# Optimization experiments

Measured on AMD Instinct MI355X. Metric: run time of the kernel, lower is better.

Reference implementation:

```python
import jax, jax.numpy as jnp
import numpy as np

RADIUS = 0.1
NSAMPLE = 32
NUM_KP = 15
KP_EXTENT = 1.0
DENSITY_PARAM = 5.0
EXTENT = 2.0 * KP_EXTENT * RADIUS / DENSITY_PARAM  # 0.04
K_RADIUS = 1.5 * EXTENT                            # 0.06
C_IN, C_OUT = 64, 128
BN_EPS = 1e-5


def make_kernel_points():
    # Deterministic stand-in for create_kernel_points: first point at center
    # ('center' fixed mode), remaining points quasi-uniform in a ball of K_RADIUS.
    rs = np.random.RandomState(0)
    d = rs.randn(NUM_KP - 1, 3)
    d /= np.linalg.norm(d, axis=1, keepdims=True) + 1e-9
    r = rs.rand(NUM_KP - 1, 1) ** (1.0 / 3.0)
    pts = np.concatenate([np.zeros((1, 3)), d * r * K_RADIUS], axis=0)
    return jnp.asarray(pts, dtype=jnp.float32)  # [K, 3]


def ball_group(query_xyz, support_xyz, support_mask, radius, nsample):
    """Masked ordered ball query. Returns idx [B,N1,S] int32 and mask [B,N1,S] float."""
    # [B, N1, N2] squared distances (dominant memory traffic)
    d2 = jnp.sum((query_xyz[:, :, None, :] - support_xyz[:, None, :, :]) ** 2, axis=-1)
    valid = (d2 < radius * radius) & (support_mask[:, None, :] > 0)
    order = jnp.cumsum(valid.astype(jnp.int32), axis=-1) - 1  # rank among valid, per row
    in_cap = valid & (order < nsample)
    slot = jnp.where(in_cap, order, nsample)  # overflow -> dump slot
    B, N1, N2 = d2.shape
    j = jnp.broadcast_to(jnp.arange(N2, dtype=jnp.int32), (B, N1, N2))
    b = jnp.arange(B)[:, None, None]
    n = jnp.arange(N1)[None, :, None]
    idx = jnp.zeros((B, N1, nsample + 1), jnp.int32).at[b, n, slot].set(j)[..., :nsample]
    cnt = jnp.sum(in_cap.astype(jnp.int32), axis=-1)  # [B, N1]
    nb_mask = jnp.arange(nsample)[None, None, :] < cnt[:, :, None]
    idx = jnp.where(nb_mask, idx, idx[:, :, :1])  # pad with first neighbor
    return idx, nb_mask.astype(jnp.float32)


def setup_inputs() -> dict:
    key = jax.random.key(0)
    ks = jax.random.split(key, 6)
    B, N1, N2 = 4, 2048, 8192
    query_xyz = jax.random.uniform(ks[0], (B, N1, 3), dtype=jnp.float32)
    support_xyz = jax.random.uniform(ks[1], (B, N2, 3), dtype=jnp.float32)
    query_mask = jnp.ones((B, N1), jnp.float32)
    support_mask = jnp.ones((B, N2), jnp.float32)
    support_features = jax.random.normal(ks[2], (B, C_IN, N2), dtype=jnp.float32)
    kernel_weights = jax.random.normal(ks[3], (NUM_KP, C_IN), dtype=jnp.float32) * (1.0 / np.sqrt(C_IN))
    W_out = jax.random.normal(ks[4], (C_OUT, C_IN), dtype=jnp.float32) * (1.0 / np.sqrt(C_IN))
    gamma = jnp.ones((C_OUT,), jnp.float32)
    beta = jnp.zeros((C_OUT,), jnp.float32)
    return {
        "query_xyz": query_xyz, "support_xyz": support_xyz,
        "query_mask": query_mask, "support_mask": support_mask,
        "support_features": support_features, "K_points": make_kernel_points(),
        "kernel_weights": kernel_weights, "W_out": W_out,
        "gamma": gamma, "beta": beta,
    }


def reference(query_xyz, support_xyz, query_mask, support_mask, support_features,
              K_points, kernel_weights, W_out, gamma, beta):
    idx, nb_mask = ball_group(query_xyz, support_xyz, support_mask, RADIUS, NSAMPLE)
    # gather neighbor features: [B, N2, C] -> [B, N1, S, C]
    feats_t = jnp.transpose(support_features, (0, 2, 1))
    nbr_feats = jnp.take_along_axis(feats_t[:, None, :, :],
                                    idx[:, :, :, None], axis=2)  # [B,N1,S,C]
    # grouped relative positions: [B, N1, S, 3]
    grouped_xyz = jnp.take_along_axis(support_xyz[:, None, :, :],
                                      idx[:, :, :, None], axis=2)
    rel_pos = grouped_xyz - query_xyz[:, :, None, :]
    # kernel-point distances: [B, N1, S, K]
    diff = rel_pos[:, :, :, None, :] - K_points[None, None, None, :, :]
    sq_d = jnp.sum(diff * diff, axis=-1)
    # linear influence, then permute to [B, N1, K, S]
    w = jnp.clip(1.0 - jnp.sqrt(sq_d) / EXTENT, 0.0, None)
    w = jnp.transpose(w, (0, 1, 3, 2))
    feature_mask = nb_mask + (1.0 - query_mask[:, :, None])  # [B,N1,S]
    w = w * feature_mask[:, :, None, :]
    # weighted sum over neighbors: [B, N1, K, C]
    weighted = jnp.einsum('bnks,bnsc->bnkc', w, nbr_feats)
    out = jnp.sum(weighted * kernel_weights[None, None, :, :], axis=2)  # [B,N1,C]
    out = jnp.transpose(out, (0, 2, 1))  # [B, C_in, N1]
    # out_conv: 1x1 conv (no bias) + BatchNorm1d (training-mode batch stats) + ReLU
    out = jnp.einsum('oc,bcn->bon', W_out, out)  # [B, C_out, N1]
    mean = jnp.mean(out, axis=(0, 2), keepdims=True)
    var = jnp.mean((out - mean) ** 2, axis=(0, 2), keepdims=True)
    out = (out - mean) * jax.lax.rsqrt(var + BN_EPS)
    out = out * gamma[None, :, None] + beta[None, :, None]
    return jax.nn.relu(out)
```

## Files before the change

### kernel.cpp

```cpp
#include <hip/hip_runtime.h>
#include <stdint.h>
#include <limits.h>

#define BATCH 4
#define N1D   2048
#define N2D   8192
#define NSAMP 32
#define NKP   15
#define CIN   64
#define COUT  128

#define RAD2    0.01f
#define INV_EXT 25.0f
#define BN_EPS  1e-5f
#define CMARG   0.1000001f

#define NWAVE 4
#define QPB   NWAVE
#define NCELL 1000
#define MAXC  80
#define NPF   4

#define WS_BPTS   131072
#define WS_FEATT  262144
#define WS_OUT2   2367488
#define WS_CS     3416064
#define WS_CNT    3420160
#define WS_CUR    3424256

__device__ __forceinline__ int cell_of(float x, float y, float z) {
  int cx = (int)(x*10.f); cx = cx < 0 ? 0 : (cx > 9 ? 9 : cx);
  int cy = (int)(y*10.f); cy = cy < 0 ? 0 : (cy > 9 ? 9 : cy);
  int cz = (int)(z*10.f); cz = cz < 0 ? 0 : (cz > 9 ? 9 : cz);
  return (cx*10 + cy)*10 + cz;
}

__global__ __launch_bounds__(256) void pg_prep(
    const float* __restrict__ sxyz, const float* __restrict__ smask,
    const float* __restrict__ sfeat, float* __restrict__ featT,
    int* __restrict__ cellCnt)
{
  __shared__ float tile[64*65];
  const int t  = threadIdx.x;
  const int bt = blockIdx.x;

  if (bt >= 512) {
    const int idx = bt - 512;
    const int bb  = idx >> 5;
    const int i   = ((idx & 31) << 8) + t;
    if (smask[bb*N2D + i] > 0.f) {
      const float* p = sxyz + ((size_t)bb*N2D + i)*3;
      atomicAdd(&cellCnt[bb*1024 + cell_of(p[0], p[1], p[2])], 1);
    }
    return;
  }

  const int b  = bt >> 7;
  const int j0 = (bt & 127) * 64;
  const float* src = sfeat + (size_t)(b*CIN)*N2D + j0;
#pragma unroll
  for (int i = 0; i < 4; ++i) {
    const int c  = i*16 + (t >> 4);
    const int j4 = (t & 15) * 4;
    const float4 v = *(const float4*)(src + (size_t)c*N2D + j4);
    tile[c*65 + j4+0] = v.x;
    tile[c*65 + j4+1] = v.y;
    tile[c*65 + j4+2] = v.z;
    tile[c*65 + j4+3] = v.w;
  }
  __syncthreads();
  float* dstb = featT + (size_t)(b*N2D + j0) * CIN;
#pragma unroll
  for (int r = 0; r < 4; ++r) {
    const int j  = r*16 + (t >> 4);
    const int c4 = (t & 15) * 4;
    float4 v;
    v.x = tile[(c4+0)*65 + j];
    v.y = tile[(c4+1)*65 + j];
    v.z = tile[(c4+2)*65 + j];
    v.w = tile[(c4+3)*65 + j];
    *(float4*)(dstb + j*CIN + c4) = v;
  }
}

__global__ __launch_bounds__(256) void pg_binscan(
    const int* __restrict__ cellCnt, const float* __restrict__ sxyz,
    const float* __restrict__ smask, int* __restrict__ cellCur,
    float4* __restrict__ bpts, int* __restrict__ cellStart)
{
  __shared__ int off_s[NCELL+1];
  __shared__ int wsum[4];
  const int t     = threadIdx.x;
  const int lane  = t & 63;
  const int wv    = t >> 6;
  const int bb    = blockIdx.x >> 5;
  const int slice = blockIdx.x & 31;
  const int* cnt  = cellCnt + bb*1024;

  int c0 = 0, c1 = 0, c2 = 0, c3 = 0, v = 0;
  if (t < 250) {
    c0 = cnt[t*4+0]; c1 = cnt[t*4+1]; c2 = cnt[t*4+2]; c3 = cnt[t*4+3];
    v = c0 + c1 + c2 + c3;
  }
  int x = v;
#pragma unroll
  for (int off = 1; off < 64; off <<= 1) {
    int y = __shfl_up(x, off);
    if (lane >= off) x += y;
  }
  if (lane == 63) wsum[wv] = x;
  __syncthreads();
  int base = 0;
#pragma unroll
  for (int w = 0; w < 4; ++w) if (w < wv) base += wsum[w];
  const int excl = base + x - v;
  if (t < 250) {
    int o = excl;
    off_s[t*4+0] = o; o += c0;
    off_s[t*4+1] = o; o += c1;
    off_s[t*4+2] = o; o += c2;
    off_s[t*4+3] = o;
  }
  if (t == 0) off_s[NCELL] = wsum[0]+wsum[1]+wsum[2]+wsum[3];
  __syncthreads();

  if (slice == 0) {
    for (int i = t; i < NCELL+1; i += 256)
      cellStart[bb*(NCELL+1) + i] = off_s[i];
  }

  const int i = slice*256 + t;
  if (smask[bb*N2D + i] > 0.f) {
    const float* p = sxyz + ((size_t)bb*N2D + i)*3;
    const float px = p[0], py = p[1], pz = p[2];
    const int cell = cell_of(px, py, pz);
    const int pos = off_s[cell] + atomicAdd(&cellCur[bb*1024 + cell], 1);
    bpts[(size_t)bb*N2D + pos] = make_float4(px, py, pz, __int_as_float(i));
  }
}

__global__ __launch_bounds__(256) void pg_main(
    const float* __restrict__ qxyz, const float* __restrict__ qmask,
    const float4* __restrict__ bpts, const int* __restrict__ cellStart,
    const float* __restrict__ featT, const float* __restrict__ Kp,
    const float* __restrict__ KW, const float* __restrict__ Wout,
    const float* __restrict__ sxyz, float* __restrict__ out2)
{
  __shared__ __align__(16) float4 s_cand4[QPB][MAXC];
  __shared__ __align__(16) int    s_candj[QPB][MAXC];
  __shared__ __align__(16) float4 s_sel[QPB][NSAMP];
  __shared__ __align__(16) int    s_j[QPB][NSAMP];
  __shared__ __align__(16) float  s_w[QPB*NSAMP*16];
  __shared__ float                s_xq[QPB*68];

  const int t    = threadIdx.x;
  const int lane = t & 63;
  const int wv   = t >> 6;
  const int gbase = blockIdx.x * QPB;
  const int b     = gbase >> 11;
  const uint64_t lt = (1ull << lane) - 1ull;

  const int g = gbase + wv;
  const float qx = qxyz[g*3+0], qy = qxyz[g*3+1], qz = qxyz[g*3+2];

  const float4* bptsb = bpts + (size_t)b*N2D;
  int cq;
  {
    int cx0 = (int)((qx-CMARG)*10.f); if (cx0 < 0) cx0 = 0;
    int cx1 = (int)((qx+CMARG)*10.f); if (cx1 > 9) cx1 = 9;
    int cy0 = (int)((qy-CMARG)*10.f); if (cy0 < 0) cy0 = 0;
    int cy1 = (int)((qy+CMARG)*10.f); if (cy1 > 9) cy1 = 9;
    int cz0 = (int)((qz-CMARG)*10.f); if (cz0 < 0) cz0 = 0;
    int cz1 = (int)((qz+CMARG)*10.f); if (cz1 > 9) cz1 = 9;
    const int ny = cy1 - cy0 + 1;
    const int npair = (cx1 - cx0 + 1) * ny;

    int len = 0, rs = 0;
    if (lane < npair) {
      const int cx = cx0 + lane / ny;
      const int cy = cy0 + lane % ny;
      const float lox = cx*0.1f, loy = cy*0.1f;
      const float dxc = fmaxf(fmaxf(lox - qx, qx - (lox+0.1f)), 0.f);
      const float dyc = fmaxf(fmaxf(loy - qy, qy - (loy+0.1f)), 0.f);
      if (dxc*dxc + dyc*dyc < RAD2) {
        const int* csb = cellStart + b*(NCELL+1) + (cx*10 + cy)*10;
        rs  = csb[cz0];
        len = csb[cz1 + 1] - rs;
      }
    }
    int pc = len;
#pragma unroll
    for (int off = 1; off < 16; off <<= 1) {
      int y = __shfl_up(pc, off);
      if (lane >= off) pc += y;
    }
    const int tot   = __shfl(pc, 15);
    const int excl  = pc - len;
    const int sbase = rs - excl;

    int segc[9], segb[9];
#pragma unroll
    for (int e = 0; e < 9; ++e) {
      const int ce = __builtin_amdgcn_readlane(excl,  e);
      const int be = __builtin_amdgcn_readlane(sbase, e);
      segc[e] = (e < npair) ? ce : INT_MAX;
      segb[e] = (e < npair) ? be : 0;
    }

    int ccnt = 0;
    for (int base0 = 0; base0 < tot; base0 += 64*NPF) {
      float4 pt[NPF];
#pragma unroll
      for (int u = 0; u < NPF; ++u) {
        const int idx = base0 + u*64 + lane;
        if (idx < tot) {
          int bb2 = segb[0];
#pragma unroll
          for (int e = 1; e < 9; ++e) if (segc[e] <= idx) bb2 = segb[e];
          pt[u] = bptsb[bb2 + idx];
        }
      }
#pragma unroll
      for (int u = 0; u < NPF; ++u) {
        const int idx = base0 + u*64 + lane;
        bool ok = false;
        if (idx < tot) {
          const float dx = pt[u].x - qx, dy = pt[u].y - qy, dz = pt[u].z - qz;
          ok = (dx*dx + dy*dy + dz*dz) < RAD2;
        }
        const uint64_t m = __ballot(ok);
        if (ok) {
          const int pos = ccnt + __popcll(m & lt);
          if (pos < MAXC) {
            s_cand4[wv][pos] = pt[u];
            s_candj[wv][pos] = __float_as_int(pt[u].w);
          }
        }
        ccnt += (int)__popcll(m);
      }
    }
    const int C = ccnt < MAXC ? ccnt : MAXC;
    const int C4 = (C + 3) & ~3;
    if (C + lane < C4) s_candj[wv][C + lane] = INT_MAX;

    const int jA = (lane      < C) ? s_candj[wv][lane]      : INT_MAX;
    const int jB = (lane + 64 < C) ? s_candj[wv][lane + 64] : INT_MAX;
    int rA = 0, rB = 0;
    for (int e = 0; e < C4; e += 4) {
      const int4 v4 = *(const int4*)&s_candj[wv][e];
      rA += (v4.x < jA) + (v4.y < jA) + (v4.z < jA) + (v4.w < jA);
      rB += (v4.x < jB) + (v4.y < jB) + (v4.z < jB) + (v4.w < jB);
    }
    if (lane      < C && rA < NSAMP) s_sel[wv][rA] = s_cand4[wv][lane];
    if (lane + 64 < C && rB < NSAMP) s_sel[wv][rB] = s_cand4[wv][lane + 64];
    cq = C < NSAMP ? C : NSAMP;
  }

  {
    const int s    = lane & 31;
    const int half = lane >> 5;
    float4 sel;
    if (cq > 0) {
      sel = s_sel[wv][s < cq ? s : 0];
    } else {
      sel = make_float4(sxyz[(size_t)b*N2D*3+0], sxyz[(size_t)b*N2D*3+1],
                        sxyz[(size_t)b*N2D*3+2], __int_as_float(0));
    }
    if (half == 0) s_j[wv][s] = __float_as_int(sel.w);
    const float rx = sel.x - qx;
    const float ry = sel.y - qy;
    const float rz = sel.z - qz;

    float w[8];
#pragma unroll
    for (int ki = 0; ki < 8; ++ki) {
      const int k  = half*8 + ki;
      const int kc = k < NKP-1 ? k : NKP-1;
      const float dx = rx - Kp[kc*3+0];
      const float dy = ry - Kp[kc*3+1];
      const float dz = rz - Kp[kc*3+2];
      float wk = fmaxf(1.0f - sqrtf(dx*dx+dy*dy+dz*dz)*INV_EXT, 0.0f);
      w[ki] = (k < NKP) ? wk : 0.0f;
    }
    float4* wrow = (float4*)&s_w[(wv*NSAMP + s)*16 + half*8];
    wrow[0] = make_float4(w[0], w[1], w[2], w[3]);
    wrow[1] = make_float4(w[4], w[5], w[6], w[7]);
  }

  {
    float kw[16];
#pragma unroll
    for (int k = 0; k < NKP; ++k) kw[k] = KW[k*CIN + lane];
    kw[15] = 0.0f;

    const float fpad = 1.0f - qmask[g];
    const int cqs = __builtin_amdgcn_readfirstlane(cq);

    float ft[NSAMP];
#pragma unroll
    for (int s = 0; s < NSAMP; ++s) {
      const int j = __builtin_amdgcn_readfirstlane(s_j[wv][s]);
      ft[s] = featT[(size_t)(b*N2D + j)*CIN + lane];
    }

    float acc = 0.0f;
#pragma unroll
    for (int s = 0; s < NSAMP; ++s) {
      const float fm = ((s < cqs) ? 1.0f : 0.0f) + fpad;
      const float4* wp = (const float4*)&s_w[(wv*NSAMP + s)*16];
      const float4 w0 = wp[0], w1 = wp[1], w2 = wp[2], w3 = wp[3];
      float wsum;
      wsum = w0.x*kw[0];
      wsum = fmaf(w0.y, kw[1],  wsum);
      wsum = fmaf(w0.z, kw[2],  wsum);
      wsum = fmaf(w0.w, kw[3],  wsum);
      wsum = fmaf(w1.x, kw[4],  wsum);
      wsum = fmaf(w1.y, kw[5],  wsum);
      wsum = fmaf(w1.z, kw[6],  wsum);
      wsum = fmaf(w1.w, kw[7],  wsum);
      wsum = fmaf(w2.x, kw[8],  wsum);
      wsum = fmaf(w2.y, kw[9],  wsum);
      wsum = fmaf(w2.z, kw[10], wsum);
      wsum = fmaf(w2.w, kw[11], wsum);
      wsum = fmaf(w3.x, kw[12], wsum);
      wsum = fmaf(w3.y, kw[13], wsum);
      wsum = fmaf(w3.z, kw[14], wsum);
      wsum = fmaf(w3.w, kw[15], wsum);
      acc = fmaf(fm*wsum, ft[s], acc);
    }
    s_xq[wv*68 + lane] = acc;
  }
  __syncthreads();

  {
    const int n4 = t & 3;
    const int og = t >> 2;
    const int gq = gbase + n4;
    const int nn = gq & 2047;
    const float4* xr = (const float4*)&s_xq[n4*68];
    const float4* w0 = (const float4*)(Wout + (og*2+0)*CIN);
    const float4* w1 = (const float4*)(Wout + (og*2+1)*CIN);
    float a0 = 0.f, a1 = 0.f;
#pragma unroll
    for (int c4 = 0; c4 < 16; ++c4) {
      const float4 x4 = xr[c4];
      const float4 wa = w0[c4];
      const float4 wb = w1[c4];
      a0 = fmaf(wa.x, x4.x, fmaf(wa.y, x4.y, fmaf(wa.z, x4.z, fmaf(wa.w, x4.w, a0))));
      a1 = fmaf(wb.x, x4.x, fmaf(wb.y, x4.y, fmaf(wb.z, x4.z, fmaf(wb.w, x4.w, a1))));
    }
    float* ob = out2 + (size_t)(b*COUT + og*2)*N1D + nn;
    ob[0]   = a0;
    ob[N1D] = a1;
  }
}

__global__ __launch_bounds__(256) void pg_finish(
    const float* __restrict__ out2, const float* __restrict__ gamma,
    const float* __restrict__ beta, float* __restrict__ dout)
{
  __shared__ float red[8];
  __shared__ float mv[2];
  const int t  = threadIdx.x;
  const int o  = blockIdx.x & 127;
  const int bb = blockIdx.x >> 7;
  float4 f[4][2];
  float s1 = 0.f, s2 = 0.f;
#pragma unroll
  for (int r = 0; r < BATCH; ++r) {
    const float4* p = (const float4*)(out2 + (size_t)(r*COUT + o)*N1D);
#pragma unroll
    for (int i = 0; i < 2; ++i) {
      const float4 x = p[i*256 + t];
      f[r][i] = x;
      s1 += x.x + x.y + x.z + x.w;
      s2 += x.x*x.x + x.y*x.y + x.z*x.z + x.w*x.w;
    }
  }
#pragma unroll
  for (int off = 32; off; off >>= 1) {
    s1 += __shfl_xor(s1, off);
    s2 += __shfl_xor(s2, off);
  }
  const int wv = t >> 6;
  if ((t & 63) == 0) { red[wv] = s1; red[4+wv] = s2; }
  __syncthreads();
  if (t == 0) {
    const float inv = 1.0f / (float)(BATCH*N1D);
    const float mean = (red[0]+red[1]+red[2]+red[3]) * inv;
    const float var  = (red[4]+red[5]+red[6]+red[7]) * inv - mean*mean;
    mv[0] = mean;
    mv[1] = rsqrtf(var + BN_EPS);
  }
  __syncthreads();
  const float mean = mv[0];
  const float ga = gamma[o] * mv[1];
  const float be = beta[o];
  float4* dp = (float4*)(dout + (size_t)(bb*COUT + o)*N1D);
#pragma unroll
  for (int i = 0; i < 2; ++i) {
    const float4 x = f[bb][i];
    float4 y;
    y.x = fmaxf((x.x - mean)*ga + be, 0.0f);
    y.y = fmaxf((x.y - mean)*ga + be, 0.0f);
    y.z = fmaxf((x.z - mean)*ga + be, 0.0f);
    y.w = fmaxf((x.w - mean)*ga + be, 0.0f);
    dp[i*256 + t] = y;
  }
}

extern "C" void kernel_launch(void* const* d_in, const int* in_sizes, int n_in,
                              void* d_out, int out_size, void* d_ws, size_t ws_size,
                              hipStream_t stream)
{
  const float* qxyz  = (const float*)d_in[0];
  const float* sxyz  = (const float*)d_in[1];
  const float* qmask = (const float*)d_in[2];
  const float* smask = (const float*)d_in[3];
  const float* sfeat = (const float*)d_in[4];
  const float* Kp    = (const float*)d_in[5];
  const float* KW    = (const float*)d_in[6];
  const float* Wout  = (const float*)d_in[7];
  const float* gamma = (const float*)d_in[8];
  const float* beta  = (const float*)d_in[9];
  float* ws = (float*)d_ws;
  float4* bpts = (float4*)(ws + WS_BPTS);
  float* featT = ws + WS_FEATT;
  float* out2  = ws + WS_OUT2;
  int*   cellS = (int*)(ws + WS_CS);
  int*   cellC = (int*)(ws + WS_CNT);
  int*   cellU = (int*)(ws + WS_CUR);
  float* dst   = (float*)d_out;

  hipMemsetAsync(cellC, 0, 2*BATCH*1024*sizeof(int), stream);
  pg_prep   <<<640,  256, 0, stream>>>(sxyz, smask, sfeat, featT, cellC);
  pg_binscan<<<128,  256, 0, stream>>>(cellC, sxyz, smask, cellU, bpts, cellS);
  pg_main   <<<2048, 256, 0, stream>>>(qxyz, qmask, bpts, cellS, featT,
                                       Kp, KW, Wout, sxyz, out2);
  pg_finish <<<512,  256, 0, stream>>>(out2, gamma, beta, dst);
}
```

Measured before the change: 126.5 us.

## Replace scanned cell binning with fixed-capacity per-cell buckets and hoist feature gather

Support points are written straight into fixed-capacity buckets of 40 slots per grid cell during the counting pass. This removes the prefix-scan/scatter kernel, its extra memset and a launch. The ball query now walks up to 27 individual cells, each bounds-checked in 3D, instead of 9 contiguous z-column ranges, which makes segment selection per candidate costlier. The neighbour feature gather is moved ahead of the kernel-point weight computation so its memory latency can overlap that math. The risk is that any cell holding more than 40 points silently drops neighbours, so correctness depends on the input point density.

Result: no change. 124.1 us (-1.9%).

```diff
diff --git a/kernel.cpp b/kernel.cpp
--- a/kernel.cpp
+++ b/kernel.cpp
@@ -17,16 +17,14 @@
 
 #define NWAVE 4
 #define QPB   NWAVE
-#define NCELL 1000
+#define CAP   40
 #define MAXC  80
 #define NPF   4
 
-#define WS_BPTS   131072
-#define WS_FEATT  262144
-#define WS_OUT2   2367488
-#define WS_CS     3416064
-#define WS_CNT    3420160
-#define WS_CUR    3424256
+#define WS_FEATT  0
+#define WS_OUT2   2097152
+#define WS_CNT    3145728
+#define WS_BPTS   3149824
 
 __device__ __forceinline__ int cell_of(float x, float y, float z) {
   int cx = (int)(x*10.f); cx = cx < 0 ? 0 : (cx > 9 ? 9 : cx);
@@ -38,7 +36,7 @@
 __global__ __launch_bounds__(256) void pg_prep(
     const float* __restrict__ sxyz, const float* __restrict__ smask,
     const float* __restrict__ sfeat, float* __restrict__ featT,
-    int* __restrict__ cellCnt)
+    int* __restrict__ cellCnt, float4* __restrict__ bpts)
 {
   __shared__ float tile[64*65];
   const int t  = threadIdx.x;
@@ -50,7 +48,11 @@
     const int i   = ((idx & 31) << 8) + t;
     if (smask[bb*N2D + i] > 0.f) {
       const float* p = sxyz + ((size_t)bb*N2D + i)*3;
-      atomicAdd(&cellCnt[bb*1024 + cell_of(p[0], p[1], p[2])], 1);
+      const float px = p[0], py = p[1], pz = p[2];
+      const int cell = bb*1024 + cell_of(px, py, pz);
+      const int pos = atomicAdd(&cellCnt[cell], 1);
+      if (pos < CAP)
+        bpts[(size_t)cell*CAP + pos] = make_float4(px, py, pz, __int_as_float(i));
     }
     return;
   }
@@ -83,65 +85,9 @@
   }
 }
 
-__global__ __launch_bounds__(256) void pg_binscan(
-    const int* __restrict__ cellCnt, const float* __restrict__ sxyz,
-    const float* __restrict__ smask, int* __restrict__ cellCur,
-    float4* __restrict__ bpts, int* __restrict__ cellStart)
-{
-  __shared__ int off_s[NCELL+1];
-  __shared__ int wsum[4];
-  const int t     = threadIdx.x;
-  const int lane  = t & 63;
-  const int wv    = t >> 6;
-  const int bb    = blockIdx.x >> 5;
-  const int slice = blockIdx.x & 31;
-  const int* cnt  = cellCnt + bb*1024;
-
-  int c0 = 0, c1 = 0, c2 = 0, c3 = 0, v = 0;
-  if (t < 250) {
-    c0 = cnt[t*4+0]; c1 = cnt[t*4+1]; c2 = cnt[t*4+2]; c3 = cnt[t*4+3];
-    v = c0 + c1 + c2 + c3;
-  }
-  int x = v;
-#pragma unroll
-  for (int off = 1; off < 64; off <<= 1) {
-    int y = __shfl_up(x, off);
-    if (lane >= off) x += y;
-  }
-  if (lane == 63) wsum[wv] = x;
-  __syncthreads();
-  int base = 0;
-#pragma unroll
-  for (int w = 0; w < 4; ++w) if (w < wv) base += wsum[w];
-  const int excl = base + x - v;
-  if (t < 250) {
-    int o = excl;
-    off_s[t*4+0] = o; o += c0;
-    off_s[t*4+1] = o; o += c1;
-    off_s[t*4+2] = o; o += c2;
-    off_s[t*4+3] = o;
-  }
-  if (t == 0) off_s[NCELL] = wsum[0]+wsum[1]+wsum[2]+wsum[3];
-  __syncthreads();
-
-  if (slice == 0) {
-    for (int i = t; i < NCELL+1; i += 256)
-      cellStart[bb*(NCELL+1) + i] = off_s[i];
-  }
-
-  const int i = slice*256 + t;
-  if (smask[bb*N2D + i] > 0.f) {
-    const float* p = sxyz + ((size_t)bb*N2D + i)*3;
-    const float px = p[0], py = p[1], pz = p[2];
-    const int cell = cell_of(px, py, pz);
-    const int pos = off_s[cell] + atomicAdd(&cellCur[bb*1024 + cell], 1);
-    bpts[(size_t)bb*N2D + pos] = make_float4(px, py, pz, __int_as_float(i));
-  }
-}
-
 __global__ __launch_bounds__(256) void pg_main(
     const float* __restrict__ qxyz, const float* __restrict__ qmask,
-    const float4* __restrict__ bpts, const int* __restrict__ cellStart,
+    const float4* __restrict__ bpts, const int* __restrict__ cellCnt,
     const float* __restrict__ featT, const float* __restrict__ Kp,
     const float* __restrict__ KW, const float* __restrict__ Wout,
     const float* __restrict__ sxyz, float* __restrict__ out2)
@@ -163,7 +109,6 @@
   const int g = gbase + wv;
   const float qx = qxyz[g*3+0], qy = qxyz[g*3+1], qz = qxyz[g*3+2];
 
-  const float4* bptsb = bpts + (size_t)b*N2D;
   int cq;
   {
     int cx0 = (int)((qx-CMARG)*10.f); if (cx0 < 0) cx0 = 0;
@@ -172,39 +117,44 @@
     int cy1 = (int)((qy+CMARG)*10.f); if (cy1 > 9) cy1 = 9;
     int cz0 = (int)((qz-CMARG)*10.f); if (cz0 < 0) cz0 = 0;
     int cz1 = (int)((qz+CMARG)*10.f); if (cz1 > 9) cz1 = 9;
-    const int ny = cy1 - cy0 + 1;
-    const int npair = (cx1 - cx0 + 1) * ny;
-
-    int len = 0, rs = 0;
-    if (lane < npair) {
-      const int cx = cx0 + lane / ny;
-      const int cy = cy0 + lane % ny;
-      const float lox = cx*0.1f, loy = cy*0.1f;
+    const int nz  = cz1 - cz0 + 1;
+    const int nyz = (cy1 - cy0 + 1) * nz;
+    const int ncl = (cx1 - cx0 + 1) * nyz;
+
+    int len = 0, base = 0;
+    if (lane < ncl) {
+      int r = lane;
+      const int cx = cx0 + r / nyz;  r %= nyz;
+      const int cy = cy0 + r / nz;
+      const int cz = cz0 + r % nz;
+      const float lox = cx*0.1f, loy = cy*0.1f, loz = cz*0.1f;
       const float dxc = fmaxf(fmaxf(lox - qx, qx - (lox+0.1f)), 0.f);
       const float dyc = fmaxf(fmaxf(loy - qy, qy - (loy+0.1f)), 0.f);
-      if (dxc*dxc + dyc*dyc < RAD2) {
-        const int* csb = cellStart + b*(NCELL+1) + (cx*10 + cy)*10;
-        rs  = csb[cz0];
-        len = csb[cz1 + 1] - rs;
+      const float dzc = fmaxf(fmaxf(loz - qz, qz - (loz+0.1f)), 0.f);
+      if (dxc*dxc + dyc*dyc + dzc*dzc < RAD2) {
+        const int cell = b*1024 + (cx*10 + cy)*10 + cz;
+        const int cnt = cellCnt[cell];
+        len  = cnt < CAP ? cnt : CAP;
+        base = cell*CAP;
       }
     }
     int pc = len;
 #pragma unroll
-    for (int off = 1; off < 16; off <<= 1) {
+    for (int off = 1; off < 64; off <<= 1) {
       int y = __shfl_up(pc, off);
       if (lane >= off) pc += y;
     }
-    const int tot   = __shfl(pc, 15);
-    const int excl  = pc - len;
-    const int sbase = rs - excl;
-
-    int segc[9], segb[9];
-#pragma unroll
-    for (int e = 0; e < 9; ++e) {
-      const int ce = __builtin_amdgcn_readlane(excl,  e);
-      const int be = __builtin_amdgcn_readlane(sbase, e);
-      segc[e] = (e < npair) ? ce : INT_MAX;
-      segb[e] = (e < npair) ? be : 0;
+    const int tot  = __shfl(pc, 63);
+    const int excl = pc - len;
+    const int sb   = base - excl;
+
+    int segc[27], segb[27];
+#pragma unroll
+    for (int e = 0; e < 27; ++e) {
+      const int ce = __builtin_amdgcn_readlane(excl, e);
+      const int be = __builtin_amdgcn_readlane(sb,   e);
+      segc[e] = (e < ncl) ? ce : INT_MAX;
+      segb[e] = (e < ncl) ? be : 0;
     }
 
     int ccnt = 0;
@@ -216,8 +166,8 @@
         if (idx < tot) {
           int bb2 = segb[0];
 #pragma unroll
-          for (int e = 1; e < 9; ++e) if (segc[e] <= idx) bb2 = segb[e];
-          pt[u] = bptsb[bb2 + idx];
+          for (int e = 1; e < 27; ++e) if (segc[e] <= idx) bb2 = segb[e];
+          pt[u] = bpts[bb2 + idx];
         }
       }
 #pragma unroll
@@ -266,7 +216,23 @@
       sel = make_float4(sxyz[(size_t)b*N2D*3+0], sxyz[(size_t)b*N2D*3+1],
                         sxyz[(size_t)b*N2D*3+2], __int_as_float(0));
     }
-    if (half == 0) s_j[wv][s] = __float_as_int(sel.w);
+    if (half == 0) {
+      s_sel[wv][s] = sel;
+      s_j[wv][s]   = __float_as_int(sel.w);
+    }
+  }
+
+  float ft[NSAMP];
+#pragma unroll
+  for (int s = 0; s < NSAMP; ++s) {
+    const int j = __builtin_amdgcn_readfirstlane(s_j[wv][s]);
+    ft[s] = featT[(size_t)(b*N2D + j)*CIN + lane];
+  }
+
+  {
+    const int s    = lane & 31;
+    const int half = lane >> 5;
+    const float4 sel = s_sel[wv][s];
     const float rx = sel.x - qx;
     const float ry = sel.y - qy;
     const float rz = sel.z - qz;
@@ -295,13 +261,6 @@
 
     const float fpad = 1.0f - qmask[g];
     const int cqs = __builtin_amdgcn_readfirstlane(cq);
-
-    float ft[NSAMP];
-#pragma unroll
-    for (int s = 0; s < NSAMP; ++s) {
-      const int j = __builtin_amdgcn_readfirstlane(s_j[wv][s]);
-      ft[s] = featT[(size_t)(b*N2D + j)*CIN + lane];
-    }
 
     float acc = 0.0f;
 #pragma unroll
@@ -424,18 +383,15 @@
   const float* gamma = (const float*)d_in[8];
   const float* beta  = (const float*)d_in[9];
   float* ws = (float*)d_ws;
-  float4* bpts = (float4*)(ws + WS_BPTS);
-  float* featT = ws + WS_FEATT;
-  float* out2  = ws + WS_OUT2;
-  int*   cellS = (int*)(ws + WS_CS);
-  int*   cellC = (int*)(ws + WS_CNT);
-  int*   cellU = (int*)(ws + WS_CUR);
-  float* dst   = (float*)d_out;
-
-  hipMemsetAsync(cellC, 0, 2*BATCH*1024*sizeof(int), stream);
-  pg_prep   <<<640,  256, 0, stream>>>(sxyz, smask, sfeat, featT, cellC);
-  pg_binscan<<<128,  256, 0, stream>>>(cellC, sxyz, smask, cellU, bpts, cellS);
-  pg_main   <<<2048, 256, 0, stream>>>(qxyz, qmask, bpts, cellS, featT,
-                                       Kp, KW, Wout, sxyz, out2);
-  pg_finish <<<512,  256, 0, stream>>>(out2, gamma, beta, dst);
-}
+  float*  featT = ws + WS_FEATT;
+  float*  out2  = ws + WS_OUT2;
+  int*    cellC = (int*)(ws + WS_CNT);
+  float4* bpts  = (float4*)(ws + WS_BPTS);
+  float* dst    = (float*)d_out;
+
+  hipMemsetAsync(cellC, 0, BATCH*1024*sizeof(int), stream);
+  pg_prep  <<<640,  256, 0, stream>>>(sxyz, smask, sfeat, featT, cellC, bpts);
+  pg_main  <<<2048, 256, 0, stream>>>(qxyz, qmask, bpts, cellC, featT,
+                                      Kp, KW, Wout, sxyz, out2);
+  pg_finish<<<512,  256, 0, stream>>>(out2, gamma, beta, dst);
+}
```
